# Optimization experiments

Hardware: AMD Instinct MI355X
Metric: run time of the kernel (lower is better)

The kernel has to match this reference:

```python
import jax, jax.numpy as jnp
import numpy as np

H = 24  # hidden size hard-coded in TrendGRU


def setup_inputs() -> dict:
    key = jax.random.key(0)
    ks = jax.random.split(key, 7)
    B, T = 32768, 512
    s_ih = 1.0 / np.sqrt(H)
    x = jax.random.normal(ks[0], (B, T, 1), dtype=jnp.float32)
    # GRUCell params (PyTorch layout: rows ordered r, z, n)
    W_ih = jax.random.uniform(ks[1], (3 * H, 1), minval=-s_ih, maxval=s_ih, dtype=jnp.float32)
    W_hh = jax.random.uniform(ks[2], (3 * H, H), minval=-s_ih, maxval=s_ih, dtype=jnp.float32)
    b_ih = jax.random.uniform(ks[3], (3 * H,), minval=-s_ih, maxval=s_ih, dtype=jnp.float32)
    b_hh = jax.random.uniform(ks[4], (3 * H,), minval=-s_ih, maxval=s_ih, dtype=jnp.float32)
    fc_w = jax.random.uniform(ks[5], (2, H), minval=-s_ih, maxval=s_ih, dtype=jnp.float32)
    fc_b = jax.random.uniform(ks[6], (2,), minval=-s_ih, maxval=s_ih, dtype=jnp.float32)
    return {"x": x, "W_ih": W_ih, "b_ih": b_ih, "W_hh": W_hh, "b_hh": b_hh,
            "fc_w": fc_w, "fc_b": fc_b}


def _gru_scan(x, W_ih, b_ih, W_hh, b_hh):
    B = x.shape[0]
    # precompute input projections for all timesteps: (B,T,1)@(1,3H) -> (T,B,3H)
    gx = jnp.einsum('bti,gi->tbg', x, W_ih) + b_ih
    h0 = jnp.zeros((B, H), dtype=x.dtype)

    def step(h, gx_t):
        gh = h @ W_hh.T + b_hh                      # (B, 3H)
        xr, xz, xn = jnp.split(gx_t, 3, axis=-1)    # PyTorch order r, z, n
        hr, hz, hn = jnp.split(gh, 3, axis=-1)
        r = jax.nn.sigmoid(xr + hr)
        z = jax.nn.sigmoid(xz + hz)
        n = jnp.tanh(xn + r * hn)
        h_new = (1.0 - z) * n + z * h
        return h_new, None

    h_final, _ = jax.lax.scan(step, h0, gx)
    return h_final


def reference(x, W_ih, b_ih, W_hh, b_hh, fc_w, fc_b):
    h = _gru_scan(x, W_ih, b_ih, W_hh, b_hh)
    return h @ fc_w.T + fc_b  # (B, 2)
```

## Files before the change

kernel.cpp:

```cpp
#include <hip/hip_runtime.h>


#define GRU_T 512
#define HS 40
#define FS 28

typedef __attribute__((ext_vector_type(8)))  short bf16x8;
typedef __attribute__((ext_vector_type(16))) float f32x16;

__device__ __forceinline__ float bf16hi_f(float v) {
    unsigned u = __float_as_uint(v);
    u = (u + 0x7FFFu + ((u >> 16) & 1u)) & 0xFFFF0000u;
    return __uint_as_float(u);
}
__device__ __forceinline__ unsigned bf16_rne(float v) {
    unsigned u = __float_as_uint(v);
    return (u + 0x7FFFu + ((u >> 16) & 1u)) >> 16;
}
__device__ __forceinline__ float sigf(float a) {
    return __builtin_amdgcn_rcpf(1.0f + __builtin_amdgcn_exp2f(-a));
}
__device__ __forceinline__ float tnhf(float v) {
    return fmaf(-2.0f, __builtin_amdgcn_rcpf(1.0f + __builtin_amdgcn_exp2f(v)), 1.0f);
}
__device__ __forceinline__ f32x16 mfma32(bf16x8 a, bf16x8 b, f32x16 c) {
    return __builtin_amdgcn_mfma_f32_32x32x16_bf16(a, b, c, 0, 0, 0);
}

__global__ __launch_bounds__(64) void trend_gru_mfma32(
    const float* __restrict__ x,
    const float* __restrict__ W_ih,
    const float* __restrict__ b_ih,
    const float* __restrict__ W_hh,
    const float* __restrict__ b_hh,
    const float* __restrict__ fc_w,
    const float* __restrict__ fc_b,
    float* __restrict__ out)
{
    const int lane = threadIdx.x;
    const int e    = lane & 31;
    const int half = lane >> 5;
    const int elem0 = blockIdx.x * 32;

    __shared__ __align__(16) unsigned short Hlds[32 * HS];
    __shared__ __align__(16) float Flds[32 * FS];

    const float L2E = 1.4426950408889634f;

    bf16x8 A[3][2][2];
#pragma unroll
    for (int g = 0; g < 3; ++g) {
        const float sc = (g == 2) ? 2.0f * L2E : L2E;
        const int m = e;
        const bool valid = m < 24;
        const int R = g * 24 + (valid ? m : 0);
        const float wx = (g < 2 && valid) ? sc * W_ih[R] : 0.0f;
        const float bb = valid ? sc * ((g < 2) ? (b_ih[R] + b_hh[R]) : b_hh[R]) : 0.0f;
        const float wxh = bf16hi_f(wx), bbh = bf16hi_f(bb);
#pragma unroll
        for (int s = 0; s < 2; ++s) {
            bf16x8 fh, fl;
#pragma unroll
            for (int jj = 0; jj < 8; ++jj) {
                const int k = s * 16 + half * 8 + jj;
                float vh = 0.0f, vl = 0.0f;
                if (valid && k < 24) {
                    const float w  = sc * W_hh[R * 24 + k];
                    const float wh = bf16hi_f(w);
                    vh = wh; vl = w - wh;
                } else if (valid) {
                    if (k == 24 || k == 25)      vh = wxh;
                    else if (k == 26)            vh = wx - wxh;
                    else if (k == 27)            vh = bbh;
                    else if (k == 28)            vh = bb - bbh;
                }
                fh[jj] = (short)bf16_rne(vh);
                fl[jj] = (short)bf16_rne(vl);
            }
            A[g][s][0] = fh;
            A[g][s][1] = fl;
        }
    }

    float wn_s[12], bn_s[12];
#pragma unroll
    for (int s = 0; s < 12; ++s) {
        const int j = (s & 3) + 8 * (s >> 2) + 4 * half;
        wn_s[s] = 2.0f * L2E * W_ih[48 + j];
        bn_s[s] = 2.0f * L2E * b_ih[48 + j];
    }

    {
        uint2 z2; z2.x = 0; z2.y = 0;
#pragma unroll
        for (int G = 0; G < 3; ++G)
            *(uint2*)(&Hlds[e * HS + G * 8 + half * 4]) = z2;
    }

    const float* xp = x + (size_t)(elem0 + e) * GRU_T;
    float xv = xp[0];

    float h[12];
#pragma unroll
    for (int s = 0; s < 12; ++s) h[s] = 0.0f;

    const f32x16 z16 = {0.f,0.f,0.f,0.f,0.f,0.f,0.f,0.f,
                        0.f,0.f,0.f,0.f,0.f,0.f,0.f,0.f};

#pragma unroll 1
    for (int t = 0; t < GRU_T; ++t) {
        const bf16x8 B0 = *(const bf16x8*)(&Hlds[e * HS + half * 8]);
        bf16x8 B1 = *(const bf16x8*)(&Hlds[e * HS + 16]);
        {
            const unsigned uhi = bf16_rne(xv);
            const float xh = __uint_as_float(uhi << 16);
            const unsigned ulo = bf16_rne(xv - xh);
            uint4 xq;
            xq.x = uhi | (ulo << 16);
            xq.y = uhi | 0x3F800000u;
            xq.z = 0x00003F80u;
            xq.w = 0;
            if (half) B1 = *(bf16x8*)&xq;
        }
        const float xnext = xp[(t + 1 < GRU_T) ? t + 1 : t];

        f32x16 aR = mfma32(A[0][0][0], B0, z16);
        aR = mfma32(A[0][0][1], B0, aR);
        aR = mfma32(A[0][1][0], B1, aR);
        aR = mfma32(A[0][1][1], B1, aR);
        f32x16 aZ = mfma32(A[1][0][0], B0, z16);
        aZ = mfma32(A[1][0][1], B0, aZ);
        aZ = mfma32(A[1][1][0], B1, aZ);
        aZ = mfma32(A[1][1][1], B1, aZ);
        f32x16 aN = mfma32(A[2][0][0], B0, z16);
        aN = mfma32(A[2][0][1], B0, aN);
        aN = mfma32(A[2][1][0], B1, aN);
        aN = mfma32(A[2][1][1], B1, aN);

#pragma unroll
        for (int G = 0; G < 3; ++G) {
            unsigned u4[4];
#pragma unroll
            for (int q = 0; q < 4; ++q) {
                const int s = G * 4 + q;
                const float rr  = sigf(aR[s]);
                const float zz  = sigf(aZ[s]);
                const float aXv = fmaf(wn_s[s], xv, bn_s[s]);
                const float nn  = tnhf(fmaf(rr, aN[s], aXv));
                const float hn  = fmaf(zz, h[s] - nn, nn);
                h[s] = hn;
                unsigned u = __float_as_uint(hn);
                u4[q] = u + 0x7FFFu + ((u >> 16) & 1u);
            }
            uint2 d;
            d.x = __builtin_amdgcn_perm(u4[1], u4[0], 0x07060302u);
            d.y = __builtin_amdgcn_perm(u4[3], u4[2], 0x07060302u);
            *(uint2*)(&Hlds[e * HS + G * 8 + half * 4]) = d;
        }
        xv = xnext;
    }

#pragma unroll
    for (int G = 0; G < 3; ++G) {
        float4 f4;
        f4.x = h[G * 4 + 0]; f4.y = h[G * 4 + 1];
        f4.z = h[G * 4 + 2]; f4.w = h[G * 4 + 3];
        *(float4*)(&Flds[e * FS + G * 8 + half * 4]) = f4;
    }
    if (lane < 32) {
        float o0 = fc_b[0], o1 = fc_b[1];
#pragma unroll
        for (int j = 0; j < 24; ++j) {
            const float hv = Flds[lane * FS + j];
            o0 = fmaf(hv, fc_w[j],      o0);
            o1 = fmaf(hv, fc_w[24 + j], o1);
        }
        float2 o; o.x = o0; o.y = o1;
        *(float2*)(out + (size_t)(elem0 + lane) * 2) = o;
    }
}

extern "C" void kernel_launch(void* const* d_in, const int* in_sizes, int n_in,
                              void* d_out, int out_size, void* d_ws, size_t ws_size,
                              hipStream_t stream) {
    const float* x    = (const float*)d_in[0];
    const float* W_ih = (const float*)d_in[1];
    const float* b_ih = (const float*)d_in[2];
    const float* W_hh = (const float*)d_in[3];
    const float* b_hh = (const float*)d_in[4];
    const float* fc_w = (const float*)d_in[5];
    const float* fc_b = (const float*)d_in[6];
    float* out = (float*)d_out;

    const int B = in_sizes[0] / GRU_T;
    const int grid = B / 32;
    trend_gru_mfma32<<<grid, 64, 0, stream>>>(x, W_ih, b_ih, W_hh, b_hh,
                                              fc_w, fc_b, out);
}
```

Before: 476.4 us.

## Switch GRU recurrence to 16x16x32 MFMA with 16 sequences per wave

Replaces the 32x32x16 bf16 MFMA formulation, 32 sequences per wave, with 16x16x32 MFMA processing 16 sequences per wave. The full K=32 augmented vector (hidden state, x split and bias) now fits in one operand, so each gate needs two MFMAs (hi and lo weights) instead of four. Each lane also computes fewer pointwise gate elements per step, which shortens the serial per-timestep latency. The cost is twice as many waves, and the final FC projection now uses cross-lane shuffles instead of an LDS staging buffer.

```diff
diff --git a/kernel.cpp b/kernel.cpp
--- a/kernel.cpp
+++ b/kernel.cpp
@@ -3,10 +3,9 @@
 
 #define GRU_T 512
 #define HS 40
-#define FS 28
-
-typedef __attribute__((ext_vector_type(8)))  short bf16x8;
-typedef __attribute__((ext_vector_type(16))) float f32x16;
+
+typedef __attribute__((ext_vector_type(8))) short bf16x8;
+typedef __attribute__((ext_vector_type(4))) float f32x4;
 
 __device__ __forceinline__ float bf16hi_f(float v) {
     unsigned u = __float_as_uint(v);
@@ -23,11 +22,11 @@
 __device__ __forceinline__ float tnhf(float v) {
     return fmaf(-2.0f, __builtin_amdgcn_rcpf(1.0f + __builtin_amdgcn_exp2f(v)), 1.0f);
 }
-__device__ __forceinline__ f32x16 mfma32(bf16x8 a, bf16x8 b, f32x16 c) {
-    return __builtin_amdgcn_mfma_f32_32x32x16_bf16(a, b, c, 0, 0, 0);
-}
-
-__global__ __launch_bounds__(64) void trend_gru_mfma32(
+__device__ __forceinline__ f32x4 mfma16(bf16x8 a, bf16x8 b, f32x4 c) {
+    return __builtin_amdgcn_mfma_f32_16x16x32_bf16(a, b, c, 0, 0, 0);
+}
+
+__global__ __launch_bounds__(64) void trend_gru_k32(
     const float* __restrict__ x,
     const float* __restrict__ W_ih,
     const float* __restrict__ b_ih,
@@ -38,31 +37,30 @@
     float* __restrict__ out)
 {
     const int lane = threadIdx.x;
-    const int e    = lane & 31;
-    const int half = lane >> 5;
-    const int elem0 = blockIdx.x * 32;
-
-    __shared__ __align__(16) unsigned short Hlds[32 * HS];
-    __shared__ __align__(16) float Flds[32 * FS];
+    const int n    = lane & 15;
+    const int quad = lane >> 4;
+    const int elem0 = blockIdx.x * 16;
+
+    __shared__ __align__(16) unsigned short Hlds[16 * HS];
 
     const float L2E = 1.4426950408889634f;
 
-    bf16x8 A[3][2][2];
+    bf16x8 Ah[3][2], Al[3][2];
 #pragma unroll
     for (int g = 0; g < 3; ++g) {
         const float sc = (g == 2) ? 2.0f * L2E : L2E;
-        const int m = e;
-        const bool valid = m < 24;
-        const int R = g * 24 + (valid ? m : 0);
-        const float wx = (g < 2 && valid) ? sc * W_ih[R] : 0.0f;
-        const float bb = valid ? sc * ((g < 2) ? (b_ih[R] + b_hh[R]) : b_hh[R]) : 0.0f;
-        const float wxh = bf16hi_f(wx), bbh = bf16hi_f(bb);
-#pragma unroll
-        for (int s = 0; s < 2; ++s) {
+#pragma unroll
+        for (int T = 0; T < 2; ++T) {
+            const int u = T * 16 + n;
+            const bool valid = u < 24;
+            const int R = g * 24 + (valid ? u : 0);
+            const float wx = (g < 2 && valid) ? sc * W_ih[R] : 0.0f;
+            const float bb = valid ? sc * ((g < 2) ? (b_ih[R] + b_hh[R]) : b_hh[R]) : 0.0f;
+            const float wxh = bf16hi_f(wx), bbh = bf16hi_f(bb);
             bf16x8 fh, fl;
 #pragma unroll
-            for (int jj = 0; jj < 8; ++jj) {
-                const int k = s * 16 + half * 8 + jj;
+            for (int j = 0; j < 8; ++j) {
+                const int k = quad * 8 + j;
                 float vh = 0.0f, vl = 0.0f;
                 if (valid && k < 24) {
                     const float w  = sc * W_hh[R * 24 + k];
@@ -74,43 +72,44 @@
                     else if (k == 27)            vh = bbh;
                     else if (k == 28)            vh = bb - bbh;
                 }
-                fh[jj] = (short)bf16_rne(vh);
-                fl[jj] = (short)bf16_rne(vl);
+                fh[j] = (short)bf16_rne(vh);
+                fl[j] = (short)bf16_rne(vl);
             }
-            A[g][s][0] = fh;
-            A[g][s][1] = fl;
-        }
-    }
-
-    float wn_s[12], bn_s[12];
-#pragma unroll
-    for (int s = 0; s < 12; ++s) {
-        const int j = (s & 3) + 8 * (s >> 2) + 4 * half;
-        wn_s[s] = 2.0f * L2E * W_ih[48 + j];
-        bn_s[s] = 2.0f * L2E * b_ih[48 + j];
-    }
-
-    {
-        uint2 z2; z2.x = 0; z2.y = 0;
-#pragma unroll
-        for (int G = 0; G < 3; ++G)
-            *(uint2*)(&Hlds[e * HS + G * 8 + half * 4]) = z2;
-    }
-
-    const float* xp = x + (size_t)(elem0 + e) * GRU_T;
+            Ah[g][T] = fh;
+            Al[g][T] = fl;
+        }
+    }
+
+    float wn0[4], bn0[4], wn1[4], bn1[4];
+#pragma unroll
+    for (int r = 0; r < 4; ++r) {
+        const int u0 = quad * 4 + r;
+        const int u1 = 16 + quad * 4 + r;
+        const int u1c = (u1 < 24) ? u1 : 0;
+        wn0[r] = 2.0f * L2E * W_ih[48 + u0];
+        bn0[r] = 2.0f * L2E * b_ih[48 + u0];
+        wn1[r] = 2.0f * L2E * W_ih[48 + u1c];
+        bn1[r] = 2.0f * L2E * b_ih[48 + u1c];
+    }
+
+    if (lane < 16) {
+        uint4 z4u; z4u.x = z4u.y = z4u.z = z4u.w = 0;
+        uint2 z2u; z2u.x = z2u.y = 0;
+        *(uint4*)(&Hlds[lane * HS])      = z4u;
+        *(uint2*)(&Hlds[lane * HS + 8])  = z2u;
+        *(uint2*)(&Hlds[lane * HS + 12]) = z2u;
+        *(uint4*)(&Hlds[lane * HS + 16]) = z4u;
+    }
+
+    const float* xp = x + (size_t)(elem0 + n) * GRU_T;
     float xv = xp[0];
 
-    float h[12];
-#pragma unroll
-    for (int s = 0; s < 12; ++s) h[s] = 0.0f;
-
-    const f32x16 z16 = {0.f,0.f,0.f,0.f,0.f,0.f,0.f,0.f,
-                        0.f,0.f,0.f,0.f,0.f,0.f,0.f,0.f};
+    float h0[4] = {0.f, 0.f, 0.f, 0.f};
+    float h1[4] = {0.f, 0.f, 0.f, 0.f};
 
 #pragma unroll 1
     for (int t = 0; t < GRU_T; ++t) {
-        const bf16x8 B0 = *(const bf16x8*)(&Hlds[e * HS + half * 8]);
-        bf16x8 B1 = *(const bf16x8*)(&Hlds[e * HS + 16]);
+        uint4 bv = *(const uint4*)(&Hlds[n * HS + quad * 8]);
         {
             const unsigned uhi = bf16_rne(xv);
             const float xh = __uint_as_float(uhi << 16);
@@ -120,63 +119,78 @@
             xq.y = uhi | 0x3F800000u;
             xq.z = 0x00003F80u;
             xq.w = 0;
-            if (half) B1 = *(bf16x8*)&xq;
-        }
+            if (quad == 3) bv = xq;
+        }
+        const bf16x8 B = *(const bf16x8*)&bv;
         const float xnext = xp[(t + 1 < GRU_T) ? t + 1 : t];
 
-        f32x16 aR = mfma32(A[0][0][0], B0, z16);
-        aR = mfma32(A[0][0][1], B0, aR);
-        aR = mfma32(A[0][1][0], B1, aR);
-        aR = mfma32(A[0][1][1], B1, aR);
-        f32x16 aZ = mfma32(A[1][0][0], B0, z16);
-        aZ = mfma32(A[1][0][1], B0, aZ);
-        aZ = mfma32(A[1][1][0], B1, aZ);
-        aZ = mfma32(A[1][1][1], B1, aZ);
-        f32x16 aN = mfma32(A[2][0][0], B0, z16);
-        aN = mfma32(A[2][0][1], B0, aN);
-        aN = mfma32(A[2][1][0], B1, aN);
-        aN = mfma32(A[2][1][1], B1, aN);
-
-#pragma unroll
-        for (int G = 0; G < 3; ++G) {
-            unsigned u4[4];
-#pragma unroll
-            for (int q = 0; q < 4; ++q) {
-                const int s = G * 4 + q;
-                const float rr  = sigf(aR[s]);
-                const float zz  = sigf(aZ[s]);
-                const float aXv = fmaf(wn_s[s], xv, bn_s[s]);
-                const float nn  = tnhf(fmaf(rr, aN[s], aXv));
-                const float hn  = fmaf(zz, h[s] - nn, nn);
-                h[s] = hn;
+        const f32x4 z4 = {0.f, 0.f, 0.f, 0.f};
+        f32x4 aR0 = mfma16(Ah[0][0], B, z4); aR0 = mfma16(Al[0][0], B, aR0);
+        f32x4 aR1 = mfma16(Ah[0][1], B, z4); aR1 = mfma16(Al[0][1], B, aR1);
+        f32x4 aZ0 = mfma16(Ah[1][0], B, z4); aZ0 = mfma16(Al[1][0], B, aZ0);
+        f32x4 aZ1 = mfma16(Ah[1][1], B, z4); aZ1 = mfma16(Al[1][1], B, aZ1);
+        f32x4 aN0 = mfma16(Ah[2][0], B, z4); aN0 = mfma16(Al[2][0], B, aN0);
+        f32x4 aN1 = mfma16(Ah[2][1], B, z4); aN1 = mfma16(Al[2][1], B, aN1);
+
+        unsigned p0[4], p1[4];
+#pragma unroll
+        for (int r = 0; r < 4; ++r) {
+            {
+                const float rr = sigf(aR0[r]);
+                const float zz = sigf(aZ0[r]);
+                const float ax = fmaf(wn0[r], xv, bn0[r]);
+                const float nn = tnhf(fmaf(rr, aN0[r], ax));
+                const float hn = fmaf(zz, h0[r] - nn, nn);
+                h0[r] = hn;
                 unsigned u = __float_as_uint(hn);
-                u4[q] = u + 0x7FFFu + ((u >> 16) & 1u);
+                p0[r] = u + 0x7FFFu + ((u >> 16) & 1u);
             }
+            {
+                const float rr = sigf(aR1[r]);
+                const float zz = sigf(aZ1[r]);
+                const float ax = fmaf(wn1[r], xv, bn1[r]);
+                const float nn = tnhf(fmaf(rr, aN1[r], ax));
+                const float hn = fmaf(zz, h1[r] - nn, nn);
+                h1[r] = hn;
+                unsigned u = __float_as_uint(hn);
+                p1[r] = u + 0x7FFFu + ((u >> 16) & 1u);
+            }
+        }
+        {
             uint2 d;
-            d.x = __builtin_amdgcn_perm(u4[1], u4[0], 0x07060302u);
-            d.y = __builtin_amdgcn_perm(u4[3], u4[2], 0x07060302u);
-            *(uint2*)(&Hlds[e * HS + G * 8 + half * 4]) = d;
+            d.x = __builtin_amdgcn_perm(p0[1], p0[0], 0x07060302u);
+            d.y = __builtin_amdgcn_perm(p0[3], p0[2], 0x07060302u);
+            *(uint2*)(&Hlds[n * HS + quad * 4]) = d;
+        }
+        if (quad < 2) {
+            uint2 d;
+            d.x = __builtin_amdgcn_perm(p1[1], p1[0], 0x07060302u);
+            d.y = __builtin_amdgcn_perm(p1[3], p1[2], 0x07060302u);
+            *(uint2*)(&Hlds[n * HS + 16 + quad * 4]) = d;
         }
         xv = xnext;
     }
 
-#pragma unroll
-    for (int G = 0; G < 3; ++G) {
-        float4 f4;
-        f4.x = h[G * 4 + 0]; f4.y = h[G * 4 + 1];
-        f4.z = h[G * 4 + 2]; f4.w = h[G * 4 + 3];
-        *(float4*)(&Flds[e * FS + G * 8 + half * 4]) = f4;
-    }
-    if (lane < 32) {
-        float o0 = fc_b[0], o1 = fc_b[1];
-#pragma unroll
-        for (int j = 0; j < 24; ++j) {
-            const float hv = Flds[lane * FS + j];
-            o0 = fmaf(hv, fc_w[j],      o0);
-            o1 = fmaf(hv, fc_w[24 + j], o1);
-        }
-        float2 o; o.x = o0; o.y = o1;
-        *(float2*)(out + (size_t)(elem0 + lane) * 2) = o;
+    float o0 = 0.0f, o1 = 0.0f;
+#pragma unroll
+    for (int r = 0; r < 4; ++r) {
+        const int u0 = quad * 4 + r;
+        o0 = fmaf(h0[r], fc_w[u0],      o0);
+        o1 = fmaf(h0[r], fc_w[24 + u0], o1);
+    }
+    if (quad < 2) {
+#pragma unroll
+        for (int r = 0; r < 4; ++r) {
+            const int u1 = 16 + quad * 4 + r;
+            o0 = fmaf(h1[r], fc_w[u1],      o0);
+            o1 = fmaf(h1[r], fc_w[24 + u1], o1);
+        }
+    }
+    o0 += __shfl_xor(o0, 16);  o1 += __shfl_xor(o1, 16);
+    o0 += __shfl_xor(o0, 32);  o1 += __shfl_xor(o1, 32);
+    if (lane < 16) {
+        float2 o; o.x = o0 + fc_b[0]; o.y = o1 + fc_b[1];
+        *(float2*)(out + (size_t)(elem0 + n) * 2) = o;
     }
 }
 
@@ -193,7 +207,7 @@
     float* out = (float*)d_out;
 
     const int B = in_sizes[0] / GRU_T;
-    const int grid = B / 32;
-    trend_gru_mfma32<<<grid, 64, 0, stream>>>(x, W_ih, b_ih, W_hh, b_hh,
-                                              fc_w, fc_b, out);
-}
+    const int grid = B / 16;
+    trend_gru_k32<<<grid, 64, 0, stream>>>(x, W_ih, b_ih, W_hh, b_hh,
+                                           fc_w, fc_b, out);
+}
```

New measurement: 570.4 us. +19.7%, slower.
